# Performance work log

Measured on AMD Instinct MI355X. Metric: run time of the kernel, lower is better.

Reference implementation:

```python
import jax, jax.numpy as jnp
import numpy as np

B = 2
G = 256            # bev grid size per axis at this stride
STRIDE = 2
PAD = 2
EMB = 128
NPF = 64           # num_pos_feats = emb_dim // 2
LR = np.array([-51.2, -51.2, -3.0, 51.2, 51.2, 1.0], np.float32)
VS = np.array([0.2, 0.2], np.float32)
OFFSET = -128      # round(lr_min / (voxel * stride))
SQRT_DIM = float(np.sqrt(EMB))
Q = 65536
V = B * G * G


def pos2posemb2d(pos, num_pos_feats=NPF, temperature=10000.0):
    # standard interleaved sin/cos 2d position embedding (y first, then x)
    pos = pos * (2.0 * np.pi)
    dim_t = jnp.arange(num_pos_feats, dtype=jnp.float32)
    dim_t = temperature ** (2.0 * (dim_t // 2) / num_pos_feats)
    px = pos[..., 0:1] / dim_t
    py = pos[..., 1:2] / dim_t
    px = jnp.stack((jnp.sin(px[..., 0::2]), jnp.cos(px[..., 1::2])), axis=-1).reshape(pos.shape[0], -1)
    py = jnp.stack((jnp.sin(py[..., 0::2]), jnp.cos(py[..., 1::2])), axis=-1).reshape(pos.shape[0], -1)
    return jnp.concatenate((py, px), axis=-1)


def mlp(x, w1, b1, w2, b2):
    return jax.nn.relu(x @ w1 + b1) @ w2 + b2


def setup_inputs():
    key = jax.random.key(0)
    ks = jax.random.split(key, 16)
    # dense BEV grid of value centers -> value_map scatter is collision-free
    idx = jnp.arange(V)
    b = idx // (G * G)
    x = (idx % (G * G)) // G
    y = idx % G
    ctr_coor = jnp.stack([b, (x - 128) * STRIDE, (y - 128) * STRIDE], axis=-1).astype(jnp.int32)
    ctr_feat = jax.random.normal(ks[0], (V, EMB), jnp.float32)
    bq = jax.random.randint(ks[1], (Q,), 0, B).astype(jnp.float32)
    xy = jax.random.uniform(ks[2], (Q, 2), jnp.float32, -51.0, 51.0)
    ref_pts = jnp.concatenate([bq[:, None], xy], axis=1)
    s = 0.02
    p = lambda k, sh: jax.random.normal(k, sh, jnp.float32) * s
    return dict(
        ref_pts=ref_pts, ctr_coor=ctr_coor, ctr_feat=ctr_feat,
        q_w1=p(ks[3], (EMB, 2 * EMB)), q_b1=jnp.zeros((2 * EMB,), jnp.float32),
        q_w2=p(ks[4], (2 * EMB, EMB)), q_b2=jnp.zeros((EMB,), jnp.float32),
        v_w1=p(ks[5], (EMB, 2 * EMB)), v_b1=jnp.zeros((2 * EMB,), jnp.float32),
        v_w2=p(ks[6], (2 * EMB, EMB)), v_b2=jnp.zeros((EMB,), jnp.float32),
        se_wr=p(ks[7], (EMB, EMB)), se_br=jnp.zeros((EMB,), jnp.float32),
        se_we=p(ks[8], (EMB, EMB)), se_be=jnp.zeros((EMB,), jnp.float32),
    )


def _forward(ref_pts, ctr_feat, q_w1, q_b1, q_w2, q_b2, v_w1, v_b1, v_w2, v_b2,
             se_wr, se_br, se_we, se_be, ctr_coor):
    nv = ctr_feat.shape[0]
    lr = jnp.asarray(LR)
    vs = jnp.asarray(VS)
    # indices2metric: voxel center positions in meters
    ctr_xy = (ctr_coor[:, 1:].astype(jnp.float32) + 0.5) * vs
    # coor_to_indices: grid indices at current stride
    ctr_inds = ctr_coor[:, 1:] // STRIDE - OFFSET                 # (V,2) in [0,G)
    ref_coor = jnp.floor(ref_pts[:, 1:] / vs)                     # metric2indices
    ref_inds = (ref_coor / STRIDE - OFFSET).astype(jnp.int32)     # (Q,2) in [0,G)
    # normalized positions in [0,1]
    qp = (ref_pts[:, 1:] - lr[0:2]) / (lr[3:5] - lr[0:2])
    vp = (ctr_xy - lr[0:2]) / (lr[3:5] - lr[0:2])
    qpos = mlp(pos2posemb2d(qp), q_w1, q_b1, q_w2, q_b2)          # (Q,d)
    vpos = mlp(pos2posemb2d(vp), v_w1, v_b1, v_w2, v_b2)          # (V,d)
    # SELayer_Linear: gate value pos-emb by features
    gate = jax.nn.sigmoid(jax.nn.relu(ctr_feat @ se_wr + se_br) @ se_we + se_be)
    vpos = vpos * gate
    # build padded index map and gather 3x3 neighborhoods
    vmap_grid = -jnp.ones((B, G + 2 * PAD, G + 2 * PAD), jnp.int32)
    vmap_grid = vmap_grid.at[ctr_coor[:, 0], ctr_inds[:, 0] + PAD, ctr_inds[:, 1] + PAD].set(
        jnp.arange(nv, dtype=jnp.int32))
    r = jnp.arange(-1, 2)
    nbrs = jnp.stack(jnp.meshgrid(r, r, indexing='ij'), axis=-1).reshape(-1, 2)  # (9,2)
    bq = ref_pts[:, 0].astype(jnp.int32)
    nx = ref_inds[:, 0:1] + PAD + nbrs[:, 0]                      # (Q,9)
    ny = ref_inds[:, 1:2] + PAD + nbrs[:, 1]
    v_idx = vmap_grid[bq[:, None], nx, ny] + 1                    # missing -> 0 (padded zero row)
    vpos_pad = jnp.concatenate([jnp.zeros((1, EMB), vpos.dtype), vpos], axis=0)
    feat_pad = jnp.concatenate([jnp.zeros((1, EMB), ctr_feat.dtype), ctr_feat], axis=0)
    score = jnp.einsum('qd,qnd->qn', qpos, vpos_pad[v_idx]) / SQRT_DIM
    attn = jax.nn.softmax(score, axis=-1)
    return jnp.einsum('qn,qnd->qd', attn, feat_pad[v_idx])       # (Q,d)


def reference(ref_pts, ctr_coor, ctr_feat, q_w1, q_b1, q_w2, q_b2,
              v_w1, v_b1, v_w2, v_b2, se_wr, se_br, se_we, se_be):
    return _forward(ref_pts, ctr_feat, q_w1, q_b1, q_w2, q_b2,
                    v_w1, v_b1, v_w2, v_b2, se_wr, se_br, se_we, se_be, ctr_coor)
```

## Files before the change

### kernel.cpp

```cpp
#include <hip/hip_runtime.h>
#include <math.h>

#define SCALE_INV_SQRT_D 0.08838834764831844f

#define NQ 65536
#define NV 131072

typedef __attribute__((ext_vector_type(8))) short s16x8;
typedef __attribute__((ext_vector_type(4))) float f32x4;

__device__ __forceinline__ unsigned short f2bf(float f) {
    unsigned int u = __builtin_bit_cast(unsigned int, f);
    u += 0x7fffu + ((u >> 16) & 1u);
    return (unsigned short)(u >> 16);
}
__device__ __forceinline__ float bf2f(unsigned short s) {
    return __builtin_bit_cast(float, (unsigned)s << 16);
}
#define LGKM0() asm volatile("s_waitcnt lgkmcnt(0)" ::: "memory")
#define SBAR0() __builtin_amdgcn_sched_barrier(0)

__device__ __forceinline__ int kperm(int kk) {
    int i = kk & 7, gg = (kk >> 3) & 3, ks = kk >> 5;
    return (ks << 5) + ((i & 4) << 2) + (gg << 2) + (i & 3);
}

__global__ __launch_bounds__(256) void prep_kernel(
    const float* __restrict__ qw1, const float* __restrict__ qw2,
    const float* __restrict__ vw1, const float* __restrict__ vw2,
    const float* __restrict__ sewr, const float* __restrict__ sewe,
    unsigned short* __restrict__ wbuf)
{
    int i = blockIdx.x * 256 + threadIdx.x;
    float v;
    if (i < 32768)        { int li = i;          int n = li >> 7, k = li & 127;          v = qw1[k * 256 + n]; }
    else if (i < 65536)   { int li = i - 32768;  int n = li >> 8, k = kperm(li & 255);   v = qw2[k * 128 + n]; }
    else if (i < 98304)   { int li = i - 65536;  int n = li >> 7, k = li & 127;          v = vw1[k * 256 + n]; }
    else if (i < 131072)  { int li = i - 98304;  int n = li >> 8, k = kperm(li & 255);   v = vw2[k * 128 + n]; }
    else if (i < 147456)  { int li = i - 131072; int n = li >> 7, k = li & 127;          v = sewr[k * 128 + n]; }
    else                  { int li = i - 147456; int n = li >> 7, k = kperm(li & 127);   v = sewe[k * 128 + n]; }
    wbuf[i] = f2bf(v);
}

__global__ __launch_bounds__(512, 4) void se_gate_kernel(
    const float* __restrict__ ctr_feat,
    const unsigned short* __restrict__ sewrt,
    const float* __restrict__ sebr,
    const unsigned short* __restrict__ sewetp,
    const float* __restrict__ sebe,
    unsigned short* __restrict__ gate_p)
{
    __shared__ __attribute__((aligned(16))) char s_w[65536];
    const int t = threadIdx.x;
    for (int c = t; c < 4096; c += 512) {
        int b  = c * 16;
        int lb = b & 32767;
        int row = lb >> 8;
        int dst = (b & 32768) + (lb ^ ((row & 7) << 4));
        const unsigned short* src = (b < 32768) ? (sewrt + lb / 2) : (sewetp + (lb / 2));
        *(s16x8*)(s_w + dst) = *(const s16x8*)src;
    }
    __syncthreads();

    const int lane = t & 63, wid = t >> 6;
    const int r16 = lane & 15, g = lane >> 4;
    const int swz = (r16 & 7) << 4;
    const int w  = blockIdx.x * 8 + wid;
    const int s0 = w * 32;

    s16x8 fb[2][4];
    #pragma unroll
    for (int gr = 0; gr < 2; ++gr) {
        const int samp = s0 + gr * 16 + r16;
        #pragma unroll
        for (int ks = 0; ks < 4; ++ks) {
            const float* src = ctr_feat + (size_t)samp * 128 + ks * 32 + g * 8;
            f32x4 v0 = *(const f32x4*)(src);
            f32x4 v1 = *(const f32x4*)(src + 4);
            s16x8 pk;
            #pragma unroll
            for (int e = 0; e < 4; ++e) {
                pk[e]     = (short)f2bf(v0[e]);
                pk[4 + e] = (short)f2bf(v1[e]);
            }
            fb[gr][ks] = pk;
        }
    }
    s16x8 ga[2][4];
    #pragma unroll
    for (int u = 0; u < 4; ++u) {
        f32x4 a0[2], a1[2];
        #pragma unroll
        for (int gr = 0; gr < 2; ++gr) { a0[gr] = (f32x4)0.f; a1[gr] = (f32x4)0.f; }
        #pragma unroll
        for (int ks = 0; ks < 4; ++ks) {
            s16x8 w0 = *(const s16x8*)(s_w + ((((2 * u) * 16 + r16) * 256 + ks * 64 + g * 16) ^ swz));
            s16x8 w1 = *(const s16x8*)(s_w + ((((2 * u + 1) * 16 + r16) * 256 + ks * 64 + g * 16) ^ swz));
            #pragma unroll
            for (int gr = 0; gr < 2; ++gr) {
                a0[gr] = __builtin_amdgcn_mfma_f32_16x16x32_bf16(w0, fb[gr][ks], a0[gr], 0, 0, 0);
                a1[gr] = __builtin_amdgcn_mfma_f32_16x16x32_bf16(w1, fb[gr][ks], a1[gr], 0, 0, 0);
            }
        }
        f32x4 bb0 = *(const f32x4*)(sebr + 32 * u + g * 4);
        f32x4 bb1 = *(const f32x4*)(sebr + 32 * u + 16 + g * 4);
        #pragma unroll
        for (int gr = 0; gr < 2; ++gr) {
            s16x8 pk;
            #pragma unroll
            for (int r = 0; r < 4; ++r) {
                pk[r]     = (short)f2bf(fmaxf(a0[gr][r] + bb0[r], 0.f));
                pk[4 + r] = (short)f2bf(fmaxf(a1[gr][r] + bb1[r], 0.f));
            }
            ga[gr][u] = pk;
        }
    }
    #pragma unroll
    for (int n = 0; n < 8; ++n) {
        f32x4 acc[2] = {(f32x4)0.f, (f32x4)0.f};
        #pragma unroll
        for (int u = 0; u < 4; ++u) {
            s16x8 b = *(const s16x8*)(s_w + 32768 + (((n * 16 + r16) * 256 + u * 64 + g * 16) ^ swz));
            #pragma unroll
            for (int gr = 0; gr < 2; ++gr)
                acc[gr] = __builtin_amdgcn_mfma_f32_16x16x32_bf16(ga[gr][u], b, acc[gr], 0, 0, 0);
        }
        const int col = n * 16 + r16;
        const float bev = sebe[col];
        #pragma unroll
        for (int gr = 0; gr < 2; ++gr) {
            unsigned short pk[4];
            #pragma unroll
            for (int r = 0; r < 4; ++r)
                pk[r] = f2bf(1.0f / (1.0f + __expf(-(acc[gr][r] + bev))));
            *(unsigned long long*)(gate_p + (size_t)(2 * w + gr) * 2048 + col * 16 + g * 4)
                = *(const unsigned long long*)pk;
        }
    }
}

template<bool GATE>
__global__ __launch_bounds__(512, 2) void pe_mlp_kernel(
    const float* __restrict__ ref_pts,
    const int*   __restrict__ ctr_coor,
    const unsigned short* __restrict__ w1t,
    const float* __restrict__ b1,
    const unsigned short* __restrict__ w2tp,
    const float* __restrict__ b2,
    const unsigned short* __restrict__ gate_p,
    unsigned short* __restrict__ outb,
    int ntile32)
{
    __shared__ __attribute__((aligned(16))) char s_w[131072 + 32768];
    const int t = threadIdx.x;
    for (int c = t; c < 8192; c += 512) {
        int b = c * 16;
        if (b < 65536) {
            int row = b >> 8;
            *(s16x8*)(s_w + (b ^ ((row & 7) << 4))) = *(const s16x8*)(w1t + b / 2);
        } else {
            int lb = b - 65536;
            int row = lb >> 9;
            *(s16x8*)(s_w + 65536 + (lb ^ ((row & 7) << 4))) = *(const s16x8*)(w2tp + lb / 2);
        }
    }
    __syncthreads();

    const int lane = t & 63, wid = t >> 6;
    const int r16 = lane & 15, g = lane >> 4;
    const int swz = (r16 & 7) << 4;
    char* s_out = s_w + 131072 + wid * 4096;

    float b2v[8];
    #pragma unroll
    for (int n = 0; n < 8; ++n) b2v[n] = b2[n * 16 + r16];

    for (int w = blockIdx.x * 8 + wid; w < ntile32; w += gridDim.x * 8) {
        const int s0 = w * 32;

        s16x8 ape[2][4];
        #pragma unroll
        for (int gr = 0; gr < 2; ++gr) {
            const int samp = s0 + gr * 16 + r16;
            float xx, yy;
            if (GATE) {
                xx = ((float)ctr_coor[samp * 3 + 1] + 0.5f) * 0.2f;
                yy = ((float)ctr_coor[samp * 3 + 2] + 0.5f) * 0.2f;
            } else {
                xx = ref_pts[samp * 3 + 1];
                yy = ref_pts[samp * 3 + 2];
            }
            const float pnx = (xx + 51.2f) * (1.0f / 102.4f);
            const float pny = (yy + 51.2f) * (1.0f / 102.4f);
            #pragma unroll
            for (int ks = 0; ks < 4; ++ks) {
                const float p = (ks < 2) ? pny : pnx;
                s16x8 pk;
                #pragma unroll
                for (int j = 0; j < 4; ++j) {
                    float fr  = (float)(ks * 16 + g * 4 + j);
                    float rev = p * __builtin_exp2f(fr * -0.41524101186092029f);
                    float sn, cs;
                    asm("v_sin_f32 %0, %1" : "=v"(sn) : "v"(rev));
                    asm("v_cos_f32 %0, %1" : "=v"(cs) : "v"(rev));
                    pk[2 * j]     = (short)f2bf(sn);
                    pk[2 * j + 1] = (short)f2bf(cs);
                }
                ape[gr][ks] = pk;
            }
        }

        s16x8 ha[2][8];
        #pragma unroll
        for (int u = 0; u < 8; ++u) {
            f32x4 a0[2], a1[2];
            #pragma unroll
            for (int gr = 0; gr < 2; ++gr) { a0[gr] = (f32x4)0.f; a1[gr] = (f32x4)0.f; }
            #pragma unroll
            for (int ks = 0; ks < 4; ++ks) {
                s16x8 w0 = *(const s16x8*)(s_w + ((((2 * u) * 16 + r16) * 256 + ks * 64 + g * 16) ^ swz));
                s16x8 w1 = *(const s16x8*)(s_w + ((((2 * u + 1) * 16 + r16) * 256 + ks * 64 + g * 16) ^ swz));
                #pragma unroll
                for (int gr = 0; gr < 2; ++gr) {
                    a0[gr] = __builtin_amdgcn_mfma_f32_16x16x32_bf16(w0, ape[gr][ks], a0[gr], 0, 0, 0);
                    a1[gr] = __builtin_amdgcn_mfma_f32_16x16x32_bf16(w1, ape[gr][ks], a1[gr], 0, 0, 0);
                }
            }
            f32x4 bb0 = *(const f32x4*)(b1 + 32 * u + g * 4);
            f32x4 bb1 = *(const f32x4*)(b1 + 32 * u + 16 + g * 4);
            #pragma unroll
            for (int gr = 0; gr < 2; ++gr) {
                s16x8 pk;
                #pragma unroll
                for (int r = 0; r < 4; ++r) {
                    pk[r]     = (short)f2bf(fmaxf(a0[gr][r] + bb0[r], 0.f));
                    pk[4 + r] = (short)f2bf(fmaxf(a1[gr][r] + bb1[r], 0.f));
                }
                ha[gr][u] = pk;
            }
        }

        #pragma unroll
        for (int gr = 0; gr < 2; ++gr) {
            unsigned long long gk[8];
            if (GATE) {
                #pragma unroll
                for (int n = 0; n < 8; ++n)
                    gk[n] = *(const unsigned long long*)(
                        gate_p + (size_t)(2 * w + gr) * 2048 + (n * 16 + r16) * 16 + g * 4);
            }
            #pragma unroll
            for (int n = 0; n < 8; ++n) {
                f32x4 c = (f32x4)0.f;
                #pragma unroll
                for (int u = 0; u < 8; ++u) {
                    s16x8 b = *(const s16x8*)(s_w + 65536 + (((n * 16 + r16) * 512 + u * 64 + g * 16) ^ swz));
                    c = __builtin_amdgcn_mfma_f32_16x16x32_bf16(ha[gr][u], b, c, 0, 0, 0);
                }
                #pragma unroll
                for (int r = 0; r < 4; ++r) {
                    float v = c[r] + b2v[n];
                    if (GATE) v *= bf2f((unsigned short)(gk[n] >> (16 * r)));
                    *(unsigned short*)(s_out + (g * 4 + r) * 256 + ((n * 32 + r16 * 2) ^ (g << 5)))
                        = f2bf(v);
                }
            }
            LGKM0(); SBAR0();
            #pragma unroll
            for (int it = 0; it < 4; ++it) {
                int row = it * 4 + (lane >> 4);
                int cb  = (lane & 15) * 16;
                s16x8 val = *(const s16x8*)(s_out + row * 256 + (cb ^ (((row >> 2) & 3) << 5)));
                *(s16x8*)((char*)outb + (size_t)(s0 + gr * 16 + row) * 256 + cb) = val;
            }
            LGKM0(); SBAR0();
        }
    }
}

__global__ __launch_bounds__(256) void attn_kernel(
    const float* __restrict__ ref_pts,
    const unsigned short* __restrict__ qpos,
    const unsigned short* __restrict__ vposg,
    const float* __restrict__ ctr_feat,
    float* __restrict__ out)
{
    const int lane = threadIdx.x & 63;
    const int qi   = blockIdx.x * 4 + (threadIdx.x >> 6);

    const int   b = (int)ref_pts[qi * 3 + 0];
    const float x = ref_pts[qi * 3 + 1];
    const float y = ref_pts[qi * 3 + 2];
    const int xi = (int)(floorf(x / 0.2f) * 0.5f + 128.0f);
    const int yi = (int)(floorf(y / 0.2f) * 0.5f + 128.0f);

    const unsigned qp = *(const unsigned*)(qpos + (size_t)qi * 128 + lane * 2);
    const float qx = bf2f((unsigned short)(qp & 0xffffu));
    const float qy = bf2f((unsigned short)(qp >> 16));

    float  sc[9];
    float2 fv[9];
    #pragma unroll
    for (int n = 0; n < 9; ++n) {
        const int nx = xi + n / 3 - 1;
        const int ny = yi + n % 3 - 1;
        const bool valid = ((unsigned)nx < 256u) && ((unsigned)ny < 256u);
        float  s = 0.f;
        float2 f = {0.f, 0.f};
        if (valid) {
            const int idx = (b << 16) + (nx << 8) + ny;
            const unsigned vp = *(const unsigned*)(vposg + (size_t)idx * 128 + lane * 2);
            f = *(const float2*)(ctr_feat + (size_t)idx * 128 + lane * 2);
            s = qx * bf2f((unsigned short)(vp & 0xffffu)) + qy * bf2f((unsigned short)(vp >> 16));
        }
        sc[n] = s;
        fv[n] = f;
    }

    #pragma unroll
    for (int off = 32; off > 0; off >>= 1) {
        #pragma unroll
        for (int n = 0; n < 9; ++n)
            sc[n] += __shfl_xor(sc[n], off, 64);
    }

    float m = -1e30f;
    #pragma unroll
    for (int n = 0; n < 9; ++n) {
        sc[n] *= SCALE_INV_SQRT_D;
        m = fmaxf(m, sc[n]);
    }
    float e[9], denom = 0.f;
    #pragma unroll
    for (int n = 0; n < 9; ++n) {
        e[n] = __expf(sc[n] - m);
        denom += e[n];
    }
    const float inv = 1.0f / denom;

    float2 o = {0.f, 0.f};
    #pragma unroll
    for (int n = 0; n < 9; ++n) {
        const float w = e[n] * inv;
        o.x += w * fv[n].x;
        o.y += w * fv[n].y;
    }
    *(float2*)(out + (size_t)qi * 128 + lane * 2) = o;
}

extern "C" void kernel_launch(void* const* d_in, const int* in_sizes, int n_in,
                              void* d_out, int out_size, void* d_ws, size_t ws_size,
                              hipStream_t stream) {
    const float* ref_pts  = (const float*)d_in[0];
    const int*   ctr_coor = (const int*)d_in[1];
    const float* ctr_feat = (const float*)d_in[2];
    const float* q_w1 = (const float*)d_in[3];
    const float* q_b1 = (const float*)d_in[4];
    const float* q_w2 = (const float*)d_in[5];
    const float* q_b2 = (const float*)d_in[6];
    const float* v_w1 = (const float*)d_in[7];
    const float* v_b1 = (const float*)d_in[8];
    const float* v_w2 = (const float*)d_in[9];
    const float* v_b2 = (const float*)d_in[10];
    const float* se_wr = (const float*)d_in[11];
    const float* se_br = (const float*)d_in[12];
    const float* se_we = (const float*)d_in[13];
    const float* se_be = (const float*)d_in[14];

    unsigned short* wbuf   = (unsigned short*)d_ws;
    unsigned short* vposg  = wbuf + 163840;
    unsigned short* qposb  = vposg + (size_t)NV * 128;
    unsigned short* gate_p = qposb + (size_t)NQ * 128;

    const unsigned short* qw1t   = wbuf;
    const unsigned short* qw2tp  = wbuf + 32768;
    const unsigned short* vw1t   = wbuf + 65536;
    const unsigned short* vw2tp  = wbuf + 98304;
    const unsigned short* sewrt  = wbuf + 131072;
    const unsigned short* sewetp = wbuf + 147456;

    prep_kernel<<<640, 256, 0, stream>>>(q_w1, q_w2, v_w1, v_w2, se_wr, se_we, wbuf);

    se_gate_kernel<<<512, 512, 0, stream>>>(
        ctr_feat, sewrt, se_br, sewetp, se_be, gate_p);

    pe_mlp_kernel<false><<<256, 512, 0, stream>>>(
        ref_pts, nullptr, qw1t, q_b1, qw2tp, q_b2, nullptr, qposb, NQ / 32);

    pe_mlp_kernel<true><<<256, 512, 0, stream>>>(
        nullptr, ctr_coor, vw1t, v_b1, vw2tp, v_b2, gate_p, vposg, NV / 32);

    attn_kernel<<<NQ / 4, 256, 0, stream>>>(
        ref_pts, qposb, vposg, ctr_feat, (float*)d_out);
}
```

Baseline: 205.3 us.

## Sort queries by spatial bucket and gather bf16 features in attention

Measured after the change: 223.4 us. 8.9% more time.

```diff
diff --git a/kernel.cpp b/kernel.cpp
--- a/kernel.cpp
+++ b/kernel.cpp
@@ -5,6 +5,7 @@
 
 #define NQ 65536
 #define NV 131072
+#define NBKT 2048
 
 typedef __attribute__((ext_vector_type(8))) short s16x8;
 typedef __attribute__((ext_vector_type(4))) float f32x4;
@@ -42,13 +43,60 @@
     wbuf[i] = f2bf(v);
 }
 
+__global__ __launch_bounds__(256) void sort_zero_kernel(int* __restrict__ counts) {
+    counts[blockIdx.x * 256 + threadIdx.x] = 0;
+}
+
+__global__ __launch_bounds__(256) void sort_count_kernel(
+    const float* __restrict__ ref_pts, int* __restrict__ counts,
+    unsigned short* __restrict__ qb)
+{
+    int qi = blockIdx.x * 256 + threadIdx.x;
+    int b = (int)ref_pts[qi * 3 + 0];
+    float x = ref_pts[qi * 3 + 1], y = ref_pts[qi * 3 + 2];
+    int xi = (int)(floorf(x * 5.0f) * 0.5f + 128.0f);
+    int yi = (int)(floorf(y * 5.0f) * 0.5f + 128.0f);
+    int bucket = (b << 10) | ((xi >> 3) << 5) | (yi >> 3);
+    qb[qi] = (unsigned short)bucket;
+    atomicAdd(&counts[bucket], 1);
+}
+
+__global__ __launch_bounds__(1024) void sort_scan_kernel(
+    const int* __restrict__ counts, int* __restrict__ offs)
+{
+    __shared__ int a[NBKT], b[NBKT];
+    const int t = threadIdx.x;
+    int c0 = counts[t], c1 = counts[t + 1024];
+    a[t] = c0; a[t + 1024] = c1;
+    __syncthreads();
+    int* src = a; int* dst = b;
+    for (int d = 1; d < NBKT; d <<= 1) {
+        dst[t]        = src[t]        + ((t >= d)        ? src[t - d]        : 0);
+        dst[t + 1024] = src[t + 1024] + ((t + 1024 >= d) ? src[t + 1024 - d] : 0);
+        __syncthreads();
+        int* tmp = src; src = dst; dst = tmp;
+    }
+    offs[t]        = src[t] - c0;
+    offs[t + 1024] = src[t + 1024] - c1;
+}
+
+__global__ __launch_bounds__(256) void sort_scatter_kernel(
+    const unsigned short* __restrict__ qb, int* __restrict__ offs,
+    int* __restrict__ perm)
+{
+    int qi = blockIdx.x * 256 + threadIdx.x;
+    int pos = atomicAdd(&offs[qb[qi]], 1);
+    perm[pos] = qi;
+}
+
 __global__ __launch_bounds__(512, 4) void se_gate_kernel(
     const float* __restrict__ ctr_feat,
     const unsigned short* __restrict__ sewrt,
     const float* __restrict__ sebr,
     const unsigned short* __restrict__ sewetp,
     const float* __restrict__ sebe,
-    unsigned short* __restrict__ gate_p)
+    unsigned short* __restrict__ gate_p,
+    unsigned short* __restrict__ featb)
 {
     __shared__ __attribute__((aligned(16))) char s_w[65536];
     const int t = threadIdx.x;
@@ -84,6 +132,7 @@
                 pk[4 + e] = (short)f2bf(v1[e]);
             }
             fb[gr][ks] = pk;
+            *(s16x8*)(featb + (size_t)samp * 128 + ks * 32 + g * 8) = pk;
         }
     }
     s16x8 ga[2][4];
@@ -280,19 +329,20 @@
 
 __global__ __launch_bounds__(256) void attn_kernel(
     const float* __restrict__ ref_pts,
+    const int* __restrict__ perm,
     const unsigned short* __restrict__ qpos,
     const unsigned short* __restrict__ vposg,
-    const float* __restrict__ ctr_feat,
+    const unsigned short* __restrict__ featb,
     float* __restrict__ out)
 {
     const int lane = threadIdx.x & 63;
-    const int qi   = blockIdx.x * 4 + (threadIdx.x >> 6);
+    const int qi   = perm[blockIdx.x * 4 + (threadIdx.x >> 6)];
 
     const int   b = (int)ref_pts[qi * 3 + 0];
     const float x = ref_pts[qi * 3 + 1];
     const float y = ref_pts[qi * 3 + 2];
-    const int xi = (int)(floorf(x / 0.2f) * 0.5f + 128.0f);
-    const int yi = (int)(floorf(y / 0.2f) * 0.5f + 128.0f);
+    const int xi = (int)(floorf(x * 5.0f) * 0.5f + 128.0f);
+    const int yi = (int)(floorf(y * 5.0f) * 0.5f + 128.0f);
 
     const unsigned qp = *(const unsigned*)(qpos + (size_t)qi * 128 + lane * 2);
     const float qx = bf2f((unsigned short)(qp & 0xffffu));
@@ -310,7 +360,9 @@
         if (valid) {
             const int idx = (b << 16) + (nx << 8) + ny;
             const unsigned vp = *(const unsigned*)(vposg + (size_t)idx * 128 + lane * 2);
-            f = *(const float2*)(ctr_feat + (size_t)idx * 128 + lane * 2);
+            const unsigned fp = *(const unsigned*)(featb + (size_t)idx * 128 + lane * 2);
+            f.x = bf2f((unsigned short)(fp & 0xffffu));
+            f.y = bf2f((unsigned short)(fp >> 16));
             s = qx * bf2f((unsigned short)(vp & 0xffffu)) + qy * bf2f((unsigned short)(vp >> 16));
         }
         sc[n] = s;
@@ -371,6 +423,10 @@
     unsigned short* vposg  = wbuf + 163840;
     unsigned short* qposb  = vposg + (size_t)NV * 128;
     unsigned short* gate_p = qposb + (size_t)NQ * 128;
+    unsigned short* featb  = gate_p + (size_t)NV * 128;
+    int*            counts = (int*)(featb + (size_t)NV * 128);
+    int*            perm   = counts + NBKT;
+    unsigned short* qb     = (unsigned short*)(perm + NQ);
 
     const unsigned short* qw1t   = wbuf;
     const unsigned short* qw2tp  = wbuf + 32768;
@@ -381,8 +437,13 @@
 
     prep_kernel<<<640, 256, 0, stream>>>(q_w1, q_w2, v_w1, v_w2, se_wr, se_we, wbuf);
 
+    sort_zero_kernel<<<NBKT / 256, 256, 0, stream>>>(counts);
+    sort_count_kernel<<<NQ / 256, 256, 0, stream>>>(ref_pts, counts, qb);
+    sort_scan_kernel<<<1, 1024, 0, stream>>>(counts, counts);
+    sort_scatter_kernel<<<NQ / 256, 256, 0, stream>>>(qb, counts, perm);
+
     se_gate_kernel<<<512, 512, 0, stream>>>(
-        ctr_feat, sewrt, se_br, sewetp, se_be, gate_p);
+        ctr_feat, sewrt, se_br, sewetp, se_be, gate_p, featb);
 
     pe_mlp_kernel<false><<<256, 512, 0, stream>>>(
         ref_pts, nullptr, qw1t, q_b1, qw2tp, q_b2, nullptr, qposb, NQ / 32);
@@ -391,5 +452,5 @@
         nullptr, ctr_coor, vw1t, v_b1, vw2tp, v_b2, gate_p, vposg, NV / 32);
 
     attn_kernel<<<NQ / 4, 256, 0, stream>>>(
-        ref_pts, qposb, vposg, ctr_feat, (float*)d_out);
-}
+        ref_pts, perm, qposb, vposg, featb, (float*)d_out);
+}
```
